# Kernel optimization log

Hardware: AMD Instinct MI355X
Metric: run time of the kernel (lower is better)

## Reference

```python
import jax, jax.numpy as jnp
import numpy as np

N_STEPS = 2   # n_steps; n_head = 1 (module is only consistent for a single head)
NEG_SLOPE = 0.2


def setup_inputs() -> dict:
    key = jax.random.key(0)
    ks = jax.random.split(key, 6)
    B, C, N = 8, 2048, 2048  # N must equal input_dim (coefs*out broadcast requirement)
    s = 1.0 / np.sqrt(C).astype(np.float32)
    x = jax.random.normal(ks[0], (B, C, N), jnp.float32)
    Wa = jax.random.normal(ks[1], (C, C), jnp.float32) * s   # conv1x1, no bias
    Wb = jax.random.normal(ks[2], (C,), jnp.float32) * s     # conv1x1 -> 1 channel
    bb = jnp.zeros((1,), jnp.float32)
    Wc = jax.random.normal(ks[3], (C,), jnp.float32) * s
    bc = jnp.zeros((1,), jnp.float32)
    bias = jnp.zeros((C,), jnp.float32)                      # self.bias (zeros)
    return dict(x=x, Wa=Wa, Wb=Wb, bb=bb, Wc=Wc, bc=bc, bias=bias)


def _head_attention(out, Wa, Wb, bb, Wc, bc, bias):
    # dropout p=0.0 -> identity
    h = jnp.einsum('oc,bcn->bon', Wa, out)            # [B,C,N] conv1x1 projection
    t1 = jnp.einsum('c,bcn->bn', Wb, h) + bb          # [B,N]
    t2 = jnp.einsum('c,bcn->bn', Wc, h) + bc          # [B,N]
    z = t1[:, None, :] + t2[:, :, None]               # [B,N,N] additive outer-sum
    z = jnp.where(z >= 0, z, NEG_SLOPE * z)           # leaky_relu(0.2)
    # torch F.softmax with no dim on a 3D tensor uses legacy dim=0 (batch dim)
    coefs = jax.nn.softmax(z, axis=0)
    re = coefs * h + bias                             # bias broadcasts over last axis
    return re                                         # [B,N,N] (== [B,C,N] since N==C)


def reference(x, Wa, Wb, bb, Wc, bc, bias):
    out = x
    for _ in range(N_STEPS):
        # n_head == 1: stack of one head then mean is the head itself
        out = _head_attention(out, Wa, Wb, bb, Wc, bc, bias)
    return out
```

## Files before the change

kernel.cpp:

```cpp
#include <hip/hip_runtime.h>
#include <hip/hip_bf16.h>

typedef unsigned short ushort_t;
typedef __attribute__((ext_vector_type(8))) short bf16x8;
typedef __attribute__((ext_vector_type(4))) float f32x4;
typedef __attribute__((ext_vector_type(8))) unsigned short u16x8;
typedef __attribute__((ext_vector_type(4))) unsigned short u16x4;

#define NDIM 2048
#define BDIM 8

__device__ __forceinline__ float bf2f(unsigned short u) {
  union { unsigned int i; float f; } v; v.i = ((unsigned int)u) << 16; return v.f;
}
__device__ __forceinline__ unsigned short f2bf(float f) {
  union { float f; unsigned int i; } v; v.f = f;
  unsigned int x = v.i;
  x += 0x7fffu + ((x >> 16) & 1u);
  return (unsigned short)(x >> 16);
}

__device__ __forceinline__ void gload16(const void* g, void* l) {
  __builtin_amdgcn_global_load_lds(
      (const __attribute__((address_space(1))) void*)g,
      (__attribute__((address_space(3))) void*)l,
      16, 0, 0);
}

__global__ __launch_bounds__(256) void convert_bf16(const float* __restrict__ src,
                                                    unsigned short* __restrict__ dst, int n) {
  int i = (blockIdx.x * 256 + threadIdx.x) * 4;
  if (i < n) {
    f32x4 v = *(const f32x4*)&src[i];
    u16x4 w;
    #pragma unroll
    for (int k = 0; k < 4; ++k) w[k] = f2bf(v[k]);
    *(u16x4*)&dst[i] = w;
  }
}

__global__ __launch_bounds__(256) void transpose_convert(const float* __restrict__ x,
                                                         unsigned short* __restrict__ dst) {
  __shared__ float tile[64][65];
  const int b  = blockIdx.z;
  const int n0 = blockIdx.x * 64;
  const int c0 = blockIdx.y * 64;
  const int tr = threadIdx.x >> 4;
  const int tc = threadIdx.x & 15;
  const float* src = x + ((size_t)b * NDIM + c0) * NDIM + n0;
  #pragma unroll
  for (int p = 0; p < 4; ++p) {
    int r = p * 16 + tr;
    f32x4 v = *(const f32x4*)&src[(size_t)r * NDIM + tc * 4];
    #pragma unroll
    for (int k = 0; k < 4; ++k) tile[r][tc * 4 + k] = v[k];
  }
  __syncthreads();
  unsigned short* d = dst + ((size_t)b * NDIM + n0) * NDIM + c0;
  #pragma unroll
  for (int p = 0; p < 4; ++p) {
    int r = p * 16 + tr;
    u16x4 w;
    #pragma unroll
    for (int k = 0; k < 4; ++k) w[k] = f2bf(tile[tc * 4 + k][r]);
    *(u16x4*)&d[(size_t)r * NDIM + tc * 4] = w;
  }
}

__global__ __launch_bounds__(256) void weff1(const float* __restrict__ Wa,
                                             const float* __restrict__ Wb,
                                             const float* __restrict__ Wc,
                                             float* __restrict__ part) {
  int c  = blockIdx.x * 256 + threadIdx.x;
  int o0 = blockIdx.y * 128;
  float ab = 0.f, ac = 0.f;
  for (int o = o0; o < o0 + 128; ++o) {
    float w = Wa[(size_t)o * NDIM + c];
    ab = fmaf(Wb[o], w, ab);
    ac = fmaf(Wc[o], w, ac);
  }
  part[(size_t)(blockIdx.y * 2 + 0) * NDIM + c] = ab;
  part[(size_t)(blockIdx.y * 2 + 1) * NDIM + c] = ac;
}
__global__ __launch_bounds__(256) void weff2(const float* __restrict__ part,
                                             float* __restrict__ wbe, float* __restrict__ wce) {
  int c = blockIdx.x * 256 + threadIdx.x;
  float ab = 0.f, ac = 0.f;
  #pragma unroll
  for (int i = 0; i < 16; ++i) {
    ab += part[(size_t)(i * 2 + 0) * NDIM + c];
    ac += part[(size_t)(i * 2 + 1) * NDIM + c];
  }
  wbe[c] = ab; wce[c] = ac;
}

__global__ __launch_bounds__(256) void t_kernel(const unsigned short* __restrict__ curT,
                                                const float* __restrict__ wbe,
                                                const float* __restrict__ wce,
                                                const float* __restrict__ bb,
                                                const float* __restrict__ bc,
                                                float* __restrict__ t1, float* __restrict__ t2) {
  int row  = blockIdx.x * 4 + (threadIdx.x >> 6);
  int lane = threadIdx.x & 63;
  const unsigned short* r = curT + (size_t)row * NDIM;
  float a1 = 0.f, a2 = 0.f;
  #pragma unroll
  for (int p = 0; p < 4; ++p) {
    int c0 = p * 512 + lane * 8;
    u16x8 v = *(const u16x8*)&r[c0];
    f32x4 w1a = *(const f32x4*)&wbe[c0];
    f32x4 w1b = *(const f32x4*)&wbe[c0 + 4];
    f32x4 w2a = *(const f32x4*)&wce[c0];
    f32x4 w2b = *(const f32x4*)&wce[c0 + 4];
    #pragma unroll
    for (int j = 0; j < 4; ++j) {
      float xv = bf2f(v[j]);
      a1 = fmaf(w1a[j], xv, a1);
      a2 = fmaf(w2a[j], xv, a2);
    }
    #pragma unroll
    for (int j = 0; j < 4; ++j) {
      float xv = bf2f(v[4 + j]);
      a1 = fmaf(w1b[j], xv, a1);
      a2 = fmaf(w2b[j], xv, a2);
    }
  }
  #pragma unroll
  for (int off = 32; off > 0; off >>= 1) {
    a1 += __shfl_xor(a1, off);
    a2 += __shfl_xor(a2, off);
  }
  if (lane == 0) { t1[row] = a1 + bb[0]; t2[row] = a2 + bc[0]; }
}

__global__ __launch_bounds__(256) void s_kernel(const float* __restrict__ t1,
                                                const float* __restrict__ t2,
                                                float* __restrict__ S) {
  int n = blockIdx.x * 256 + threadIdx.x;
  int o = blockIdx.y;
  float acc = 0.f;
  #pragma unroll
  for (int b = 0; b < BDIM; ++b) {
    float z = t1[b * NDIM + n] + t2[b * NDIM + o];
    z = z >= 0.f ? z : 0.2f * z;
    acc += __expf(z);
  }
  S[(size_t)o * NDIM + n] = __logf(acc);
}

__global__ __launch_bounds__(512, 2) void gemm_fused(
    const unsigned short* __restrict__ A,
    const unsigned short* __restrict__ Bt,
    const float* __restrict__ t1, const float* __restrict__ t2,
    const float* __restrict__ S,  const float* __restrict__ bias,
    unsigned short* __restrict__ outT,
    float* __restrict__ outF,
    int write_f32) {
  __shared__ __align__(16) unsigned short sbuf[4 * 16384];

  const int tid  = threadIdx.x;
  const int lane = tid & 63;
  const int w    = tid >> 6;
  const int wr   = w >> 2;
  const int wc   = w & 3;
  const int bn0  = blockIdx.x * 256;
  const int bm0  = blockIdx.y * 256;
  const int bz   = blockIdx.z;
  const unsigned short* Bb = Bt + (size_t)bz * NDIM * NDIM;

  f32x4 acc[8][4];
  #pragma unroll
  for (int m = 0; m < 8; ++m)
    #pragma unroll
    for (int n = 0; n < 4; ++n) acc[m][n] = (f32x4){0.f, 0.f, 0.f, 0.f};

  const int sr = lane >> 2;
  const int sc = lane & 3;
  const int r0 = (w * 2 + 0) * 16 + sr;
  const int r1 = (w * 2 + 1) * 16 + sr;
  const int sg = sc ^ ((r0 >> 1) & 3);
  const unsigned short* a0 = A  + (size_t)(bm0 + r0) * NDIM + sg * 8;
  const unsigned short* a1 = A  + (size_t)(bm0 + r1) * NDIM + sg * 8;
  const unsigned short* b0 = Bb + (size_t)(bn0 + r0) * NDIM + sg * 8;
  const unsigned short* b1 = Bb + (size_t)(bn0 + r1) * NDIM + sg * 8;

  auto stageA = [&](int kt, int buf) {
    gload16(a0 + kt, &sbuf[buf * 16384 + (w * 2 + 0) * 512]);
    gload16(a1 + kt, &sbuf[buf * 16384 + (w * 2 + 1) * 512]);
  };
  auto stageB = [&](int kt, int buf) {
    gload16(b0 + kt, &sbuf[buf * 16384 + 8192 + (w * 2 + 0) * 512]);
    gload16(b1 + kt, &sbuf[buf * 16384 + 8192 + (w * 2 + 1) * 512]);
  };

  const int fr = lane & 15;
  const int fs = lane >> 4;
  const int sp = (fs ^ ((fr >> 1) & 3)) * 8;

  stageA(0, 0);  stageB(0, 0);
  stageA(32, 1); stageB(32, 1);
  stageA(64, 2); stageB(64, 2);
  asm volatile("s_waitcnt vmcnt(8)" ::: "memory");
  __builtin_amdgcn_s_barrier();

  for (int t4 = 0; t4 < 64; t4 += 4) {
    #pragma unroll
    for (int u = 0; u < 4; ++u) {
      const int t  = t4 + u;
      const int cb = u;
      const int nb = (u + 3) & 3;
      const int tc = (t + 3 > 63) ? 63 : (t + 3);
      const int ktn = tc * 32;
      const unsigned short* Ab = &sbuf[cb * 16384];
      const unsigned short* Bl = &sbuf[cb * 16384 + 8192];

      stageA(ktn, nb);
      stageB(ktn, nb);

      bf16x8 av0[4], bv[4], av1[4];
      #pragma unroll
      for (int m = 0; m < 4; ++m)
        av0[m] = *(const bf16x8*)&Ab[(wr * 128 + m * 16 + fr) * 32 + sp];
      #pragma unroll
      for (int n = 0; n < 4; ++n)
        bv[n] = *(const bf16x8*)&Bl[(wc * 64 + n * 16 + fr) * 32 + sp];
      __builtin_amdgcn_sched_barrier(0);
      #pragma unroll
      for (int m = 0; m < 4; ++m)
        av1[m] = *(const bf16x8*)&Ab[(wr * 128 + (m + 4) * 16 + fr) * 32 + sp];
      __builtin_amdgcn_sched_barrier(0);

      asm volatile("s_waitcnt lgkmcnt(4)" ::: "memory");
      __builtin_amdgcn_sched_barrier(0);
      __builtin_amdgcn_s_setprio(1);
      #pragma unroll
      for (int m = 0; m < 4; ++m)
        #pragma unroll
        for (int n = 0; n < 4; ++n)
          acc[m][n] = __builtin_amdgcn_mfma_f32_16x16x32_bf16(av0[m], bv[n], acc[m][n], 0, 0, 0);
      __builtin_amdgcn_s_setprio(0);
      __builtin_amdgcn_sched_barrier(0);

      asm volatile("s_waitcnt lgkmcnt(0)" ::: "memory");
      __builtin_amdgcn_sched_barrier(0);
      __builtin_amdgcn_s_setprio(1);
      #pragma unroll
      for (int m = 0; m < 4; ++m)
        #pragma unroll
        for (int n = 0; n < 4; ++n)
          acc[m + 4][n] = __builtin_amdgcn_mfma_f32_16x16x32_bf16(av1[m], bv[n], acc[m + 4][n], 0, 0, 0);
      __builtin_amdgcn_s_setprio(0);
      __builtin_amdgcn_sched_barrier(0);

      asm volatile("s_waitcnt vmcnt(8)" ::: "memory");
      __builtin_amdgcn_s_barrier();
    }
  }

  float* sT1f = (float*)&sbuf[0];
  float* sT2f = sT1f + 256;
  if (tid < 256) sT1f[tid] = t1[bz * NDIM + bn0 + tid];
  else           sT2f[tid - 256] = t2[bz * NDIM + bm0 + (tid - 256)];
  __syncthreads();

  const int lr4 = fs * 4;
  #pragma unroll
  for (int m = 0; m < 8; ++m) {
    #pragma unroll
    for (int n = 0; n < 4; ++n) {
      const int oo = wr * 128 + m * 16 + lr4;
      const int nn = wc * 64 + n * 16 + fr;
      const int o  = bm0 + oo;
      const int ng = bn0 + nn;
      const float tz1  = sT1f[nn];
      const float bval = bias[ng];
      if (write_f32) {
        #pragma unroll
        for (int r = 0; r < 4; ++r) {
          float z = tz1 + sT2f[oo + r];
          z = z >= 0.f ? z : 0.2f * z;
          float coef = __expf(z - S[(size_t)(o + r) * NDIM + ng]);
          outF[(size_t)bz * NDIM * NDIM + (size_t)(o + r) * NDIM + ng] =
              fmaf(coef, acc[m][n][r], bval);
        }
      } else {
        u16x4 wv;
        #pragma unroll
        for (int r = 0; r < 4; ++r) {
          float z = tz1 + sT2f[oo + r];
          z = z >= 0.f ? z : 0.2f * z;
          float coef = __expf(z - S[(size_t)(o + r) * NDIM + ng]);
          wv[r] = f2bf(fmaf(coef, acc[m][n][r], bval));
        }
        *(u16x4*)&outT[(size_t)bz * NDIM * NDIM + (size_t)ng * NDIM + o] = wv;
      }
    }
  }
}

extern "C" void kernel_launch(void* const* d_in, const int* in_sizes, int n_in,
                              void* d_out, int out_size, void* d_ws, size_t ws_size,
                              hipStream_t stream) {
  const float* x    = (const float*)d_in[0];
  const float* Wa   = (const float*)d_in[1];
  const float* Wb   = (const float*)d_in[2];
  const float* bb   = (const float*)d_in[3];
  const float* Wc   = (const float*)d_in[4];
  const float* bc   = (const float*)d_in[5];
  const float* bias = (const float*)d_in[6];
  float* out = (float*)d_out;

  char* ws = (char*)d_ws;
  unsigned short* curA = (unsigned short*)ws; ws += (size_t)BDIM * NDIM * NDIM * 2;
  unsigned short* curB = (unsigned short*)ws; ws += (size_t)BDIM * NDIM * NDIM * 2;
  unsigned short* WaB  = (unsigned short*)ws; ws += (size_t)NDIM * NDIM * 2;
  float* t1   = (float*)ws; ws += (size_t)BDIM * NDIM * 4;
  float* t2   = (float*)ws; ws += (size_t)BDIM * NDIM * 4;
  float* wbe  = (float*)ws; ws += NDIM * 4;
  float* wce  = (float*)ws; ws += NDIM * 4;
  float* part = (float*)ws; ws += (size_t)32 * NDIM * 4;
  float* S    = (float*)ws; ws += (size_t)NDIM * NDIM * 4;

  convert_bf16<<<4096, 256, 0, stream>>>(Wa, WaB, NDIM * NDIM);
  transpose_convert<<<dim3(32, 32, BDIM), 256, 0, stream>>>(x, curA);
  weff1<<<dim3(8, 16), 256, 0, stream>>>(Wa, Wb, Wc, part);
  weff2<<<8, 256, 0, stream>>>(part, wbe, wce);

  for (int step = 0; step < 2; ++step) {
    const unsigned short* cur = step ? curB : curA;
    t_kernel<<<(BDIM * NDIM) / 4, 256, 0, stream>>>(cur, wbe, wce, bb, bc, t1, t2);
    s_kernel<<<dim3(NDIM / 256, NDIM), 256, 0, stream>>>(t1, t2, S);
    gemm_fused<<<dim3(8, 8, BDIM), 512, 0, stream>>>(
        WaB, cur, t1, t2, S, bias, curB, out, step);
  }
}
```

Before: 387.0 us.

## Double-buffer MFMA register fragments to overlap LDS reads with matrix math

Restructures the GEMM main loop so the LDS fragment reads for the next k-tile are issued between the MFMA batches of the current tile, using two register fragment sets in ping-pong. The global-to-LDS staging moves to the end of each iteration and the vmcnt wait drops to 4 to match the new issue order. The goal is to hide LDS read latency behind MFMA execution rather than stalling on lgkmcnt before each compute batch. In exchange it doubles fragment register usage, which may lower occupancy, and it depends on the buffer rotation and wait counts being exactly right.

```diff
diff --git a/kernel.cpp b/kernel.cpp
--- a/kernel.cpp
+++ b/kernel.cpp
@@ -197,62 +197,76 @@
   const int fs = lane >> 4;
   const int sp = (fs ^ ((fr >> 1) & 3)) * 8;
 
+  bf16x8 avA[8], bvA[4], avB[8], bvB[4];
+
   stageA(0, 0);  stageB(0, 0);
   stageA(32, 1); stageB(32, 1);
   stageA(64, 2); stageB(64, 2);
-  asm volatile("s_waitcnt vmcnt(8)" ::: "memory");
+  asm volatile("s_waitcnt vmcnt(4)" ::: "memory");
   __builtin_amdgcn_s_barrier();
+  #pragma unroll
+  for (int m = 0; m < 8; ++m)
+    avA[m] = *(const bf16x8*)&sbuf[(wr * 128 + m * 16 + fr) * 32 + sp];
+  #pragma unroll
+  for (int n = 0; n < 4; ++n)
+    bvA[n] = *(const bf16x8*)&sbuf[8192 + (wc * 64 + n * 16 + fr) * 32 + sp];
 
   for (int t4 = 0; t4 < 64; t4 += 4) {
     #pragma unroll
     for (int u = 0; u < 4; ++u) {
       const int t  = t4 + u;
-      const int cb = u;
       const int nb = (u + 3) & 3;
       const int tc = (t + 3 > 63) ? 63 : (t + 3);
       const int ktn = tc * 32;
-      const unsigned short* Ab = &sbuf[cb * 16384];
-      const unsigned short* Bl = &sbuf[cb * 16384 + 8192];
-
-      stageA(ktn, nb);
-      stageB(ktn, nb);
-
-      bf16x8 av0[4], bv[4], av1[4];
-      #pragma unroll
-      for (int m = 0; m < 4; ++m)
-        av0[m] = *(const bf16x8*)&Ab[(wr * 128 + m * 16 + fr) * 32 + sp];
-      #pragma unroll
-      for (int n = 0; n < 4; ++n)
-        bv[n] = *(const bf16x8*)&Bl[(wc * 64 + n * 16 + fr) * 32 + sp];
-      __builtin_amdgcn_sched_barrier(0);
-      #pragma unroll
-      for (int m = 0; m < 4; ++m)
-        av1[m] = *(const bf16x8*)&Ab[(wr * 128 + (m + 4) * 16 + fr) * 32 + sp];
-      __builtin_amdgcn_sched_barrier(0);
-
-      asm volatile("s_waitcnt lgkmcnt(4)" ::: "memory");
-      __builtin_amdgcn_sched_barrier(0);
+      const unsigned short* Yb = &sbuf[((u + 1) & 3) * 16384];
+      const bool do_reads = (u < 3) || (t4 < 60);
+
+      bf16x8 (&Xav)[8] = (u & 1) ? avB : avA;
+      bf16x8 (&Xbv)[4] = (u & 1) ? bvB : bvA;
+      bf16x8 (&Yav)[8] = (u & 1) ? avA : avB;
+      bf16x8 (&Ybv)[4] = (u & 1) ? bvA : bvB;
+
+      asm volatile("s_waitcnt lgkmcnt(0)" ::: "memory");
+      __builtin_amdgcn_sched_barrier(0);
+
       __builtin_amdgcn_s_setprio(1);
       #pragma unroll
       for (int m = 0; m < 4; ++m)
         #pragma unroll
         for (int n = 0; n < 4; ++n)
-          acc[m][n] = __builtin_amdgcn_mfma_f32_16x16x32_bf16(av0[m], bv[n], acc[m][n], 0, 0, 0);
+          acc[m][n] = __builtin_amdgcn_mfma_f32_16x16x32_bf16(Xav[m], Xbv[n], acc[m][n], 0, 0, 0);
       __builtin_amdgcn_s_setprio(0);
       __builtin_amdgcn_sched_barrier(0);
 
-      asm volatile("s_waitcnt lgkmcnt(0)" ::: "memory");
-      __builtin_amdgcn_sched_barrier(0);
+      if (do_reads) {
+        #pragma unroll
+        for (int m = 0; m < 4; ++m)
+          Yav[m] = *(const bf16x8*)&Yb[(wr * 128 + m * 16 + fr) * 32 + sp];
+        #pragma unroll
+        for (int n = 0; n < 4; ++n)
+          Ybv[n] = *(const bf16x8*)&Yb[8192 + (wc * 64 + n * 16 + fr) * 32 + sp];
+      }
+      __builtin_amdgcn_sched_barrier(0);
+
       __builtin_amdgcn_s_setprio(1);
       #pragma unroll
       for (int m = 0; m < 4; ++m)
         #pragma unroll
         for (int n = 0; n < 4; ++n)
-          acc[m + 4][n] = __builtin_amdgcn_mfma_f32_16x16x32_bf16(av1[m], bv[n], acc[m + 4][n], 0, 0, 0);
+          acc[m + 4][n] = __builtin_amdgcn_mfma_f32_16x16x32_bf16(Xav[m + 4], Xbv[n], acc[m + 4][n], 0, 0, 0);
       __builtin_amdgcn_s_setprio(0);
       __builtin_amdgcn_sched_barrier(0);
 
-      asm volatile("s_waitcnt vmcnt(8)" ::: "memory");
+      if (do_reads) {
+        #pragma unroll
+        for (int m = 0; m < 4; ++m)
+          Yav[m + 4] = *(const bf16x8*)&Yb[(wr * 128 + (m + 4) * 16 + fr) * 32 + sp];
+      }
+      __builtin_amdgcn_sched_barrier(0);
+
+      stageA(ktn, nb);
+      stageB(ktn, nb);
+      asm volatile("s_waitcnt vmcnt(4)" ::: "memory");
       __builtin_amdgcn_s_barrier();
     }
   }
```

New measurement: 529.5 us. +36.8%, slower.

## Restructure GEMM main loop into 8-phase double-buffered schedule with K=64 tiles

Applied to the files above, without the earlier changes.

Replaces the 4-stage ring of K=32 tiles with two LDS buffers of K=64 tiles. Each tile is split into A and B halves that are loaded in sub-pieces interleaved with four MFMA quadrant phases, and the LDS swizzle changes to an 8-chunk XOR pattern. The goal is finer overlap of global-to-LDS loads, LDS reads and MFMA work, with fewer iterations and barriers per unit of K. In exchange it adds more barriers per iteration and depends on delicate vmcnt accounting, so a mistake there could cause stalls or races.

```diff
diff --git a/kernel.cpp b/kernel.cpp
--- a/kernel.cpp
+++ b/kernel.cpp
@@ -156,7 +156,7 @@
     unsigned short* __restrict__ outT,
     float* __restrict__ outF,
     int write_f32) {
-  __shared__ __align__(16) unsigned short sbuf[4 * 16384];
+  __shared__ __align__(16) unsigned short sbuf[65536];
 
   const int tid  = threadIdx.x;
   const int lane = tid & 63;
@@ -174,88 +174,112 @@
     #pragma unroll
     for (int n = 0; n < 4; ++n) acc[m][n] = (f32x4){0.f, 0.f, 0.f, 0.f};
 
-  const int sr = lane >> 2;
-  const int sc = lane & 3;
-  const int r0 = (w * 2 + 0) * 16 + sr;
-  const int r1 = (w * 2 + 1) * 16 + sr;
-  const int sg = sc ^ ((r0 >> 1) & 3);
-  const unsigned short* a0 = A  + (size_t)(bm0 + r0) * NDIM + sg * 8;
-  const unsigned short* a1 = A  + (size_t)(bm0 + r1) * NDIM + sg * 8;
-  const unsigned short* b0 = Bb + (size_t)(bn0 + r0) * NDIM + sg * 8;
-  const unsigned short* b1 = Bb + (size_t)(bn0 + r1) * NDIM + sg * 8;
-
-  auto stageA = [&](int kt, int buf) {
-    gload16(a0 + kt, &sbuf[buf * 16384 + (w * 2 + 0) * 512]);
-    gload16(a1 + kt, &sbuf[buf * 16384 + (w * 2 + 1) * 512]);
-  };
-  auto stageB = [&](int kt, int buf) {
-    gload16(b0 + kt, &sbuf[buf * 16384 + 8192 + (w * 2 + 0) * 512]);
-    gload16(b1 + kt, &sbuf[buf * 16384 + 8192 + (w * 2 + 1) * 512]);
+  const int sst   = (lane & 7) ^ (lane >> 3);
+  const int srowl = lane >> 3;
+  const int kk0 = w * 2, kk1 = w * 2 + 1;
+  const int rA0 = (kk0 >> 3) * 128 + (kk0 & 7) * 8;
+  const int rA1 = (kk1 >> 3) * 128 + (kk1 & 7) * 8;
+  const int rB0 = (kk0 >> 2) * 64 + (kk0 & 3) * 8;
+  const int rB1 = (kk1 >> 2) * 64 + (kk1 & 3) * 8;
+  const unsigned short* aG0 = A  + (size_t)(bm0 + rA0 + srowl) * NDIM + sst * 8;
+  const unsigned short* aG1 = A  + (size_t)(bm0 + rA1 + srowl) * NDIM + sst * 8;
+  const unsigned short* bG0 = Bb + (size_t)(bn0 + rB0 + srowl) * NDIM + sst * 8;
+  const unsigned short* bG1 = Bb + (size_t)(bn0 + rB1 + srowl) * NDIM + sst * 8;
+  const int aL0 = rA0 * 64, aL1 = rA1 * 64;
+  const int bL0 = 16384 + rB0 * 64, bL1 = 16384 + rB1 * 64;
+
+  auto stA = [&](int T, int h, int d) {
+    gload16(aG0 + (size_t)h * 64 * NDIM + T * 64, &sbuf[d * 32768 + aL0 + h * 4096]);
+    gload16(aG1 + (size_t)h * 64 * NDIM + T * 64, &sbuf[d * 32768 + aL1 + h * 4096]);
+  };
+  auto stB = [&](int T, int h, int d) {
+    gload16(bG0 + (size_t)h * 32 * NDIM + T * 64, &sbuf[d * 32768 + bL0 + h * 2048]);
+    gload16(bG1 + (size_t)h * 32 * NDIM + T * 64, &sbuf[d * 32768 + bL1 + h * 2048]);
   };
 
   const int fr = lane & 15;
   const int fs = lane >> 4;
-  const int sp = (fs ^ ((fr >> 1) & 3)) * 8;
-
-  stageA(0, 0);  stageB(0, 0);
-  stageA(32, 1); stageB(32, 1);
-  stageA(64, 2); stageB(64, 2);
-  asm volatile("s_waitcnt vmcnt(8)" ::: "memory");
+  const int sl0 = ((fs) ^ (fr & 7)) * 8;
+  const int sl1 = ((4 + fs) ^ (fr & 7)) * 8;
+  const int aOff = (wr * 128 + fr) * 64;
+  const int bOff = 16384 + (wc * 64 + fr) * 64;
+
+  bf16x8 a0[4][2], a1f[4][2], b0[2][2], b1[2][2];
+
+  auto rdA = [&](bf16x8 (&dst)[4][2], int d, int mh) {
+    const int base = d * 32768 + aOff + mh * 4096;
+    #pragma unroll
+    for (int m = 0; m < 4; ++m) {
+      dst[m][0] = *(const bf16x8*)&sbuf[base + m * 1024 + sl0];
+      dst[m][1] = *(const bf16x8*)&sbuf[base + m * 1024 + sl1];
+    }
+  };
+  auto rdB = [&](bf16x8 (&dst)[2][2], int d, int nh) {
+    const int base = d * 32768 + bOff + nh * 2048;
+    #pragma unroll
+    for (int n = 0; n < 2; ++n) {
+      dst[n][0] = *(const bf16x8*)&sbuf[base + n * 1024 + sl0];
+      dst[n][1] = *(const bf16x8*)&sbuf[base + n * 1024 + sl1];
+    }
+  };
+
+  auto quad = [&](bf16x8 (&af)[4][2], bf16x8 (&bf)[2][2], int mo, int no) {
+    #pragma unroll
+    for (int m = 0; m < 4; ++m)
+      #pragma unroll
+      for (int n = 0; n < 2; ++n)
+        #pragma unroll
+        for (int ks = 0; ks < 2; ++ks)
+          acc[mo + m][no + n] =
+              __builtin_amdgcn_mfma_f32_16x16x32_bf16(af[m][ks], bf[n][ks], acc[mo + m][no + n], 0, 0, 0);
+  };
+
+  auto phase_open = [&]() {
+    __builtin_amdgcn_sched_barrier(0);
+    __builtin_amdgcn_s_barrier();
+    asm volatile("s_waitcnt lgkmcnt(0)" ::: "memory");
+    __builtin_amdgcn_sched_barrier(0);
+    __builtin_amdgcn_s_setprio(1);
+  };
+  auto phase_close = [&](bool vm) {
+    __builtin_amdgcn_s_setprio(0);
+    __builtin_amdgcn_sched_barrier(0);
+    if (vm) asm volatile("s_waitcnt vmcnt(6)" ::: "memory");
+    __builtin_amdgcn_s_barrier();
+  };
+
+  stA(0, 0, 0); stB(0, 0, 0); stB(0, 1, 0); stA(0, 1, 0);
+  stA(1, 0, 1); stB(1, 0, 1); stB(1, 1, 1);
+  asm volatile("s_waitcnt vmcnt(6)" ::: "memory");
   __builtin_amdgcn_s_barrier();
 
-  for (int t4 = 0; t4 < 64; t4 += 4) {
-    #pragma unroll
-    for (int u = 0; u < 4; ++u) {
-      const int t  = t4 + u;
-      const int cb = u;
-      const int nb = (u + 3) & 3;
-      const int tc = (t + 3 > 63) ? 63 : (t + 3);
-      const int ktn = tc * 32;
-      const unsigned short* Ab = &sbuf[cb * 16384];
-      const unsigned short* Bl = &sbuf[cb * 16384 + 8192];
-
-      stageA(ktn, nb);
-      stageB(ktn, nb);
-
-      bf16x8 av0[4], bv[4], av1[4];
-      #pragma unroll
-      for (int m = 0; m < 4; ++m)
-        av0[m] = *(const bf16x8*)&Ab[(wr * 128 + m * 16 + fr) * 32 + sp];
-      #pragma unroll
-      for (int n = 0; n < 4; ++n)
-        bv[n] = *(const bf16x8*)&Bl[(wc * 64 + n * 16 + fr) * 32 + sp];
-      __builtin_amdgcn_sched_barrier(0);
-      #pragma unroll
-      for (int m = 0; m < 4; ++m)
-        av1[m] = *(const bf16x8*)&Ab[(wr * 128 + (m + 4) * 16 + fr) * 32 + sp];
-      __builtin_amdgcn_sched_barrier(0);
-
-      asm volatile("s_waitcnt lgkmcnt(4)" ::: "memory");
-      __builtin_amdgcn_sched_barrier(0);
-      __builtin_amdgcn_s_setprio(1);
-      #pragma unroll
-      for (int m = 0; m < 4; ++m)
-        #pragma unroll
-        for (int n = 0; n < 4; ++n)
-          acc[m][n] = __builtin_amdgcn_mfma_f32_16x16x32_bf16(av0[m], bv[n], acc[m][n], 0, 0, 0);
-      __builtin_amdgcn_s_setprio(0);
-      __builtin_amdgcn_sched_barrier(0);
-
-      asm volatile("s_waitcnt lgkmcnt(0)" ::: "memory");
-      __builtin_amdgcn_sched_barrier(0);
-      __builtin_amdgcn_s_setprio(1);
-      #pragma unroll
-      for (int m = 0; m < 4; ++m)
-        #pragma unroll
-        for (int n = 0; n < 4; ++n)
-          acc[m + 4][n] = __builtin_amdgcn_mfma_f32_16x16x32_bf16(av1[m], bv[n], acc[m + 4][n], 0, 0, 0);
-      __builtin_amdgcn_s_setprio(0);
-      __builtin_amdgcn_sched_barrier(0);
-
-      asm volatile("s_waitcnt vmcnt(8)" ::: "memory");
-      __builtin_amdgcn_s_barrier();
-    }
-  }
+  #pragma clang loop unroll(disable)
+  for (int it = 0; it < 16; ++it) {
+    const int T1 = 2 * it + 1;
+    const int T2 = (it < 15) ? 2 * it + 2 : 31;
+    const int T3 = (it < 14) ? 2 * it + 3 : 31;
+
+    rdA(a0, 0, 0); rdB(b0, 0, 0); stA(T1, 1, 1);
+    phase_open(); quad(a0, b0, 0, 0); phase_close(false);
+    rdB(b1, 0, 1); stA(T2, 0, 0);
+    phase_open(); quad(a0, b1, 0, 2); phase_close(false);
+    rdA(a1f, 0, 1); stB(T2, 0, 0);
+    phase_open(); quad(a1f, b0, 4, 0); phase_close(false);
+    stB(T2, 1, 0);
+    phase_open(); quad(a1f, b1, 4, 2); phase_close(true);
+
+    rdA(a0, 1, 0); rdB(b0, 1, 0); stA(T2, 1, 0);
+    phase_open(); quad(a0, b0, 0, 0); phase_close(false);
+    rdB(b1, 1, 1); stA(T3, 0, 1);
+    phase_open(); quad(a0, b1, 0, 2); phase_close(false);
+    rdA(a1f, 1, 1); stB(T3, 0, 1);
+    phase_open(); quad(a1f, b0, 4, 0); phase_close(false);
+    stB(T3, 1, 1);
+    phase_open(); quad(a1f, b1, 4, 2); phase_close(true);
+  }
+
+  asm volatile("s_waitcnt vmcnt(0)" ::: "memory");
+  __syncthreads();
 
   float* sT1f = (float*)&sbuf[0];
   float* sT2f = sT1f + 256;
```

Result: faster. 374.9 us (-3.1%).

## Pre-pack Wa into MFMA fragment layout and load A directly into registers

Applied to the files above, without the earlier changes.

Wa is converted into a fragment-packed bf16 layout, so each lane's A operand for the 16x16x32 MFMA is one contiguous 16-byte chunk. The GEMM now loads A straight from global memory into registers and skips LDS for A. Only B is staged through a double-buffered LDS with a new XOR swizzle and 64-wide K tiles. This cuts LDS capacity and LDS read traffic for A, at the cost of more global/L2 traffic, since each wave re-reads A fragments, and a hand-scheduled pipeline with tight vmcnt waits that is fragile to get right.

```diff
diff --git a/kernel.cpp b/kernel.cpp
--- a/kernel.cpp
+++ b/kernel.cpp
@@ -27,16 +27,19 @@
       16, 0, 0);
 }
 
-__global__ __launch_bounds__(256) void convert_bf16(const float* __restrict__ src,
-                                                    unsigned short* __restrict__ dst, int n) {
-  int i = (blockIdx.x * 256 + threadIdx.x) * 4;
-  if (i < n) {
-    f32x4 v = *(const f32x4*)&src[i];
-    u16x4 w;
-    #pragma unroll
-    for (int k = 0; k < 4; ++k) w[k] = f2bf(v[k]);
-    *(u16x4*)&dst[i] = w;
-  }
+__global__ __launch_bounds__(256) void pack_a(const float* __restrict__ Wa,
+                                              unsigned short* __restrict__ Apk) {
+  const int sub = blockIdx.x * 4 + (threadIdx.x >> 6);
+  const int l   = threadIdx.x & 63;
+  const int mt  = sub >> 6, kt = sub & 63;
+  const int fr  = l & 15, fs = l >> 4;
+  const float* src = Wa + (size_t)(mt * 16 + fr) * NDIM + kt * 32 + fs * 8;
+  f32x4 v0 = *(const f32x4*)&src[0];
+  f32x4 v1 = *(const f32x4*)&src[4];
+  u16x8 w;
+  #pragma unroll
+  for (int k = 0; k < 4; ++k) { w[k] = f2bf(v0[k]); w[4 + k] = f2bf(v1[k]); }
+  *(u16x8*)&Apk[(size_t)sub * 512 + l * 8] = w;
 }
 
 __global__ __launch_bounds__(256) void transpose_convert(const float* __restrict__ x,
@@ -149,14 +152,14 @@
 }
 
 __global__ __launch_bounds__(512, 2) void gemm_fused(
-    const unsigned short* __restrict__ A,
+    const unsigned short* __restrict__ Apk,
     const unsigned short* __restrict__ Bt,
     const float* __restrict__ t1, const float* __restrict__ t2,
     const float* __restrict__ S,  const float* __restrict__ bias,
     unsigned short* __restrict__ outT,
     float* __restrict__ outF,
     int write_f32) {
-  __shared__ __align__(16) unsigned short sbuf[4 * 16384];
+  __shared__ __align__(16) unsigned short sbuf[2][16384];
 
   const int tid  = threadIdx.x;
   const int lane = tid & 63;
@@ -174,90 +177,108 @@
     #pragma unroll
     for (int n = 0; n < 4; ++n) acc[m][n] = (f32x4){0.f, 0.f, 0.f, 0.f};
 
-  const int sr = lane >> 2;
-  const int sc = lane & 3;
-  const int r0 = (w * 2 + 0) * 16 + sr;
-  const int r1 = (w * 2 + 1) * 16 + sr;
-  const int sg = sc ^ ((r0 >> 1) & 3);
-  const unsigned short* a0 = A  + (size_t)(bm0 + r0) * NDIM + sg * 8;
-  const unsigned short* a1 = A  + (size_t)(bm0 + r1) * NDIM + sg * 8;
-  const unsigned short* b0 = Bb + (size_t)(bn0 + r0) * NDIM + sg * 8;
-  const unsigned short* b1 = Bb + (size_t)(bn0 + r1) * NDIM + sg * 8;
-
-  auto stageA = [&](int kt, int buf) {
-    gload16(a0 + kt, &sbuf[buf * 16384 + (w * 2 + 0) * 512]);
-    gload16(a1 + kt, &sbuf[buf * 16384 + (w * 2 + 1) * 512]);
+  const int sst   = (lane & 7) ^ (lane >> 3);
+  const int srowl = lane >> 3;
+  const unsigned short* bG = Bb + (size_t)(bn0 + w * 32 + srowl) * NDIM + sst * 8;
+  auto stB = [&](int T, int p, int d) {
+    gload16(bG + (size_t)p * 8 * NDIM + T * 64, &sbuf[d][(w * 32 + p * 8) * 64]);
   };
-  auto stageB = [&](int kt, int buf) {
-    gload16(b0 + kt, &sbuf[buf * 16384 + 8192 + (w * 2 + 0) * 512]);
-    gload16(b1 + kt, &sbuf[buf * 16384 + 8192 + (w * 2 + 1) * 512]);
+
+  const int fr  = lane & 15;
+  const int fs  = lane >> 4;
+  const int sl0 = ((fs) ^ (fr & 7)) * 8;
+  const int sl1 = ((4 + fs) ^ (fr & 7)) * 8;
+  const int bRow = (wc * 64 + fr) * 64;
+
+  const unsigned int mtBase = (unsigned)((bm0 >> 4) + wr * 8);
+  unsigned int aOff0[4], aOff1[4];
+  #pragma unroll
+  for (int m = 0; m < 4; ++m) {
+    aOff0[m] = ((mtBase + m) * 64u) * 1024u + lane * 16u;
+    aOff1[m] = ((mtBase + 4 + m) * 64u) * 1024u + lane * 16u;
+  }
+
+  bf16x8 Am0[4][2], Am1[4][2], bv[2][2];
+
+  auto issueA = [&](bf16x8 (&dst)[4][2], const unsigned int (&off)[4]) {
+    #pragma unroll
+    for (int m = 0; m < 4; ++m) {
+      asm volatile("global_load_dwordx4 %0, %1, %2"
+                   : "=v"(dst[m][0]) : "v"(off[m]), "s"(Apk) : "memory");
+      asm volatile("global_load_dwordx4 %0, %1, %2 offset:1024"
+                   : "=v"(dst[m][1]) : "v"(off[m]), "s"(Apk) : "memory");
+    }
   };
-
-  const int fr = lane & 15;
-  const int fs = lane >> 4;
-  const int sp = (fs ^ ((fr >> 1) & 3)) * 8;
-
-  stageA(0, 0);  stageB(0, 0);
-  stageA(32, 1); stageB(32, 1);
-  stageA(64, 2); stageB(64, 2);
+  auto rdB = [&](int nh, int d) {
+    #pragma unroll
+    for (int n = 0; n < 2; ++n) {
+      const int base = d * 16384 + bRow + (nh * 2 + n) * 16 * 64;
+      bv[n][0] = *(const bf16x8*)&sbuf[0][base + sl0];
+      bv[n][1] = *(const bf16x8*)&sbuf[0][base + sl1];
+    }
+  };
+  auto quad = [&](bf16x8 (&af)[4][2], int mo, int no) {
+    __builtin_amdgcn_s_setprio(1);
+    #pragma unroll
+    for (int m = 0; m < 4; ++m)
+      #pragma unroll
+      for (int n = 0; n < 2; ++n)
+        #pragma unroll
+        for (int ks = 0; ks < 2; ++ks)
+          acc[mo + m][no + n] = __builtin_amdgcn_mfma_f32_16x16x32_bf16(
+              af[m][ks], bv[n][ks], acc[mo + m][no + n], 0, 0, 0);
+    __builtin_amdgcn_s_setprio(0);
+    __builtin_amdgcn_sched_barrier(0);
+  };
+
+  stB(0, 0, 0); stB(0, 1, 0); stB(0, 2, 0); stB(0, 3, 0);
+  issueA(Am0, aOff0);
   asm volatile("s_waitcnt vmcnt(8)" ::: "memory");
   __builtin_amdgcn_s_barrier();
 
-  for (int t4 = 0; t4 < 64; t4 += 4) {
-    #pragma unroll
-    for (int u = 0; u < 4; ++u) {
-      const int t  = t4 + u;
-      const int cb = u;
-      const int nb = (u + 3) & 3;
-      const int tc = (t + 3 > 63) ? 63 : (t + 3);
-      const int ktn = tc * 32;
-      const unsigned short* Ab = &sbuf[cb * 16384];
-      const unsigned short* Bl = &sbuf[cb * 16384 + 8192];
-
-      stageA(ktn, nb);
-      stageB(ktn, nb);
-
-      bf16x8 av0[4], bv[4], av1[4];
+  #pragma clang loop unroll(disable)
+  for (int tt = 0; tt < 16; ++tt) {
+    const int Tn0 = 2 * tt + 1;
+    const int Tn1 = (tt == 15) ? 31 : 2 * tt + 2;
+
+    #pragma unroll
+    for (int half = 0; half < 2; ++half) {
+      const int cur = half, nxt = half ^ 1;
+      const int Tn = half ? Tn1 : Tn0;
+
+      issueA(Am1, aOff1);
       #pragma unroll
-      for (int m = 0; m < 4; ++m)
-        av0[m] = *(const bf16x8*)&Ab[(wr * 128 + m * 16 + fr) * 32 + sp];
+      for (int m = 0; m < 4; ++m) aOff1[m] += 2048u;
+      rdB(0, cur);
+      asm volatile("s_waitcnt vmcnt(8)" ::: "memory");
+      __builtin_amdgcn_sched_barrier(0);
+      quad(Am0, 0, 0);
+
+      stB(Tn, 0, nxt); stB(Tn, 1, nxt);
+      asm volatile("s_waitcnt vmcnt(2)" ::: "memory");
+      __builtin_amdgcn_sched_barrier(0);
+      quad(Am1, 4, 0);
+
+      stB(Tn, 2, nxt); stB(Tn, 3, nxt);
+      rdB(1, cur);
       #pragma unroll
-      for (int n = 0; n < 4; ++n)
-        bv[n] = *(const bf16x8*)&Bl[(wc * 64 + n * 16 + fr) * 32 + sp];
+      for (int m = 0; m < 4; ++m) aOff0[m] += 2048u;
       __builtin_amdgcn_sched_barrier(0);
-      #pragma unroll
-      for (int m = 0; m < 4; ++m)
-        av1[m] = *(const bf16x8*)&Ab[(wr * 128 + (m + 4) * 16 + fr) * 32 + sp];
+      quad(Am0, 0, 2);
+
+      issueA(Am0, aOff0);
       __builtin_amdgcn_sched_barrier(0);
-
-      asm volatile("s_waitcnt lgkmcnt(4)" ::: "memory");
-      __builtin_amdgcn_sched_barrier(0);
-      __builtin_amdgcn_s_setprio(1);
-      #pragma unroll
-      for (int m = 0; m < 4; ++m)
-        #pragma unroll
-        for (int n = 0; n < 4; ++n)
-          acc[m][n] = __builtin_amdgcn_mfma_f32_16x16x32_bf16(av0[m], bv[n], acc[m][n], 0, 0, 0);
-      __builtin_amdgcn_s_setprio(0);
-      __builtin_amdgcn_sched_barrier(0);
-
-      asm volatile("s_waitcnt lgkmcnt(0)" ::: "memory");
-      __builtin_amdgcn_sched_barrier(0);
-      __builtin_amdgcn_s_setprio(1);
-      #pragma unroll
-      for (int m = 0; m < 4; ++m)
-        #pragma unroll
-        for (int n = 0; n < 4; ++n)
-          acc[m + 4][n] = __builtin_amdgcn_mfma_f32_16x16x32_bf16(av1[m], bv[n], acc[m + 4][n], 0, 0, 0);
-      __builtin_amdgcn_s_setprio(0);
-      __builtin_amdgcn_sched_barrier(0);
+      quad(Am1, 4, 2);
 
       asm volatile("s_waitcnt vmcnt(8)" ::: "memory");
       __builtin_amdgcn_s_barrier();
     }
   }
 
-  float* sT1f = (float*)&sbuf[0];
+  asm volatile("s_waitcnt vmcnt(0)" ::: "memory");
+  __syncthreads();
+
+  float* sT1f = (float*)&sbuf[0][0];
   float* sT2f = sT1f + 256;
   if (tid < 256) sT1f[tid] = t1[bz * NDIM + bn0 + tid];
   else           sT2f[tid - 256] = t2[bz * NDIM + bm0 + (tid - 256)];
@@ -313,7 +334,7 @@
   char* ws = (char*)d_ws;
   unsigned short* curA = (unsigned short*)ws; ws += (size_t)BDIM * NDIM * NDIM * 2;
   unsigned short* curB = (unsigned short*)ws; ws += (size_t)BDIM * NDIM * NDIM * 2;
-  unsigned short* WaB  = (unsigned short*)ws; ws += (size_t)NDIM * NDIM * 2;
+  unsigned short* Apk  = (unsigned short*)ws; ws += (size_t)NDIM * NDIM * 2;
   float* t1   = (float*)ws; ws += (size_t)BDIM * NDIM * 4;
   float* t2   = (float*)ws; ws += (size_t)BDIM * NDIM * 4;
   float* wbe  = (float*)ws; ws += NDIM * 4;
@@ -321,7 +342,7 @@
   float* part = (float*)ws; ws += (size_t)32 * NDIM * 4;
   float* S    = (float*)ws; ws += (size_t)NDIM * NDIM * 4;
 
-  convert_bf16<<<4096, 256, 0, stream>>>(Wa, WaB, NDIM * NDIM);
+  pack_a<<<2048, 256, 0, stream>>>(Wa, Apk);
   transpose_convert<<<dim3(32, 32, BDIM), 256, 0, stream>>>(x, curA);
   weff1<<<dim3(8, 16), 256, 0, stream>>>(Wa, Wb, Wc, part);
   weff2<<<8, 256, 0, stream>>>(part, wbe, wce);
@@ -331,6 +352,6 @@
     t_kernel<<<(BDIM * NDIM) / 4, 256, 0, stream>>>(cur, wbe, wce, bb, bc, t1, t2);
     s_kernel<<<dim3(NDIM / 256, NDIM), 256, 0, stream>>>(t1, t2, S);
     gemm_fused<<<dim3(8, 8, BDIM), 512, 0, stream>>>(
-        WaB, cur, t1, t2, S, bias, curB, out, step);
-  }
-}
+        Apk, cur, t1, t2, S, bias, curB, out, step);
+  }
+}
```

After: 375.9 us. 1.03x faster.
